# Kernel tuning notes

Hardware: AMD Instinct MI355X
Metric: run time of the kernel (lower is better)

## Reference

```python
import jax, jax.numpy as jnp
import numpy as np

D_MODEL = 1024
NUM_HEADS = 16
HEAD_DIM = D_MODEL // NUM_HEADS


def setup_inputs() -> dict:
    key = jax.random.key(0)
    k_x, k_wqkv, k_bqkv, k_wo, k_bo = jax.random.split(key, 5)
    B, T = 2, 2048
    bound_qkv = 1.0 / np.sqrt(D_MODEL)
    bound_o = 1.0 / np.sqrt(D_MODEL)
    return {
        "x": jax.random.normal(k_x, (B, T, D_MODEL), dtype=jnp.float32),
        # stored as (in, out) for clean x @ W
        "w_qkv": jax.random.uniform(k_wqkv, (D_MODEL, 3 * D_MODEL), jnp.float32, -bound_qkv, bound_qkv),
        "b_qkv": jax.random.uniform(k_bqkv, (3 * D_MODEL,), jnp.float32, -bound_qkv, bound_qkv),
        "w_out": jax.random.uniform(k_wo, (D_MODEL, D_MODEL), jnp.float32, -bound_o, bound_o),
        "b_out": jax.random.uniform(k_bo, (D_MODEL,), jnp.float32, -bound_o, bound_o),
    }


def reference(x, w_qkv, b_qkv, w_out, b_out):
    B, T, C = x.shape
    H, Dh = NUM_HEADS, HEAD_DIM
    scale = jnp.sqrt(jnp.asarray(Dh, dtype=x.dtype))
    qkv = x @ w_qkv + b_qkv                      # [B, T, 3C]
    q, k, v = jnp.split(qkv, 3, axis=-1)         # each [B, T, C]
    # [B, T, C] -> [B, H, T, Dh]
    q = q.reshape(B, T, H, Dh).transpose(0, 2, 1, 3)
    k = k.reshape(B, T, H, Dh).transpose(0, 2, 1, 3)
    v = v.reshape(B, T, H, Dh).transpose(0, 2, 1, 3)
    scores = jnp.einsum("bhqd,bhkd->bhqk", q, k) / scale   # [B, H, T, T]
    probs = jax.nn.softmax(scores, axis=-1)
    attn = jnp.einsum("bhqk,bhkd->bhqd", probs, v)          # [B, H, T, Dh]
    attn = attn.transpose(0, 2, 1, 3).reshape(B, T, C)
    return attn @ w_out + b_out
```

## Files before the change

### kernel.cpp

```cpp
#include <hip/hip_runtime.h>
#include <stdint.h>

typedef __bf16 bf16x8 __attribute__((ext_vector_type(8)));
typedef float f32x4 __attribute__((ext_vector_type(4)));
typedef float f32x16 __attribute__((ext_vector_type(16)));
typedef unsigned short u16x8 __attribute__((ext_vector_type(8)));

#define D_MODEL 1024
#define T_SEQ 2048
#define BATCH 2
#define NHEAD 16
#define HDIM 64
#define MROWS (BATCH * T_SEQ)
#define HEADS_TOTAL (BATCH * NHEAD)
#define QKV_ELEMS (HEADS_TOTAL * T_SEQ * HDIM)

__device__ __forceinline__ unsigned short f32_to_bf16_rne(float f) {
    uint32_t u = __builtin_bit_cast(uint32_t, f);
    uint32_t r = (u + 0x7FFFu + ((u >> 16) & 1u)) >> 16;
    return (unsigned short)r;
}

__device__ __forceinline__ uint32_t pack2(float a, float b) {
    return (uint32_t)f32_to_bf16_rne(a) | ((uint32_t)f32_to_bf16_rne(b) << 16);
}

__device__ __forceinline__ void gload_lds16(const void* g, void* l) {
    __builtin_amdgcn_global_load_lds(
        (const __attribute__((address_space(1))) void*)g,
        (__attribute__((address_space(3))) void*)l, 16, 0, 0);
}

__device__ __forceinline__ f32x4 mfma_bf16(bf16x8 a, bf16x8 b, f32x4 c) {
    return __builtin_amdgcn_mfma_f32_16x16x32_bf16(a, b, c, 0, 0, 0);
}
__device__ __forceinline__ f32x16 mfma32(bf16x8 a, bf16x8 b, f32x16 c) {
    return __builtin_amdgcn_mfma_f32_32x32x16_bf16(a, b, c, 0, 0, 0);
}

__global__ void k_convert(const float4* __restrict__ in, u16x8* __restrict__ out, int n8) {
    int i = blockIdx.x * 256 + threadIdx.x;
    if (i >= n8) return;
    float4 a = in[i * 2];
    float4 b = in[i * 2 + 1];
    u16x8 r;
    r[0] = f32_to_bf16_rne(a.x); r[1] = f32_to_bf16_rne(a.y);
    r[2] = f32_to_bf16_rne(a.z); r[3] = f32_to_bf16_rne(a.w);
    r[4] = f32_to_bf16_rne(b.x); r[5] = f32_to_bf16_rne(b.y);
    r[6] = f32_to_bf16_rne(b.z); r[7] = f32_to_bf16_rne(b.w);
    out[i] = r;
}

__global__ void k_transpose_conv(const float* __restrict__ in, unsigned short* __restrict__ out,
                                 int R, int C) {
    __shared__ float tile[32][33];
    int nc = C >> 5;
    int tc0 = (blockIdx.x % nc) * 32;
    int tr0 = (blockIdx.x / nc) * 32;
    int tx = threadIdx.x & 31, ty = threadIdx.x >> 5;
#pragma unroll
    for (int i = 0; i < 4; ++i) {
        int r = ty * 4 + i;
        tile[r][tx] = in[(size_t)(tr0 + r) * C + tc0 + tx];
    }
    __syncthreads();
#pragma unroll
    for (int i = 0; i < 4; ++i) {
        int c = ty * 4 + i;
        out[(size_t)(tc0 + c) * R + tr0 + tx] = f32_to_bf16_rne(tile[tx][c]);
    }
}

template <int EPI>
__global__ __launch_bounds__(256) void k_gemm(const unsigned short* __restrict__ A,
                                              const unsigned short* __restrict__ Bt,
                                              const float* __restrict__ bias,
                                              void* __restrict__ outp,
                                              int M, int N, int K) {
    __shared__ __align__(16) unsigned short As[128 * 32];
    __shared__ __align__(16) unsigned short Bs[128 * 32];
    const int NB = N >> 7;
    int bm = blockIdx.x / NB, bn = blockIdx.x % NB;
    int tid = threadIdx.x;
    int lane = tid & 63, w = tid >> 6;
    int wr = w >> 1, wc = w & 1;
    int l15 = lane & 15, lg = lane >> 4;

    f32x4 acc[4][4] = {};

    const int nK = K >> 5;
    int c1 = tid, c2 = tid + 256;
    int r1 = c1 >> 2, o1 = (c1 & 3) * 8;
    int r2 = c2 >> 2, o2 = (c2 & 3) * 8;
    char* AsB = (char*)As;
    char* BsB = (char*)Bs;

    for (int kt = 0; kt < nK; ++kt) {
        if (kt) __syncthreads();
        int k0 = kt * 32;
        gload_lds16(A + (size_t)(bm * 128 + r1) * K + k0 + o1, AsB + w * 1024);
        gload_lds16(A + (size_t)(bm * 128 + r2) * K + k0 + o2, AsB + 4096 + w * 1024);
        gload_lds16(Bt + (size_t)(bn * 128 + r1) * K + k0 + o1, BsB + w * 1024);
        gload_lds16(Bt + (size_t)(bn * 128 + r2) * K + k0 + o2, BsB + 4096 + w * 1024);
        __syncthreads();

        bf16x8 af[4], bfr[4];
#pragma unroll
        for (int i = 0; i < 4; ++i)
            af[i] = *(const bf16x8*)(As + (wr * 64 + i * 16 + l15) * 32 + lg * 8);
#pragma unroll
        for (int j = 0; j < 4; ++j)
            bfr[j] = *(const bf16x8*)(Bs + (wc * 64 + j * 16 + l15) * 32 + lg * 8);
#pragma unroll
        for (int i = 0; i < 4; ++i)
#pragma unroll
            for (int j = 0; j < 4; ++j)
                acc[i][j] = mfma_bf16(af[i], bfr[j], acc[i][j]);
    }

    if (EPI == 1) {
        float* out = (float*)outp;
#pragma unroll
        for (int jn = 0; jn < 4; ++jn) {
            int n = bn * 128 + wc * 64 + jn * 16 + l15;
            float bv = bias[n];
#pragma unroll
            for (int i = 0; i < 4; ++i) {
#pragma unroll
                for (int j = 0; j < 4; ++j) {
                    int m = bm * 128 + wr * 64 + i * 16 + lg * 4 + j;
                    out[(size_t)m * N + n] = acc[i][jn][j] + bv;
                }
            }
        }
    } else {
        unsigned short* qkv = (unsigned short*)outp;
#pragma unroll
        for (int jn = 0; jn < 4; ++jn) {
            int n = bn * 128 + wc * 64 + jn * 16 + l15;
            float bv = bias[n];
            int part = n >> 10;
            int cc = n & 1023;
            int h = cc >> 6, d = cc & 63;
            float scale = (part == 0) ? 0.125f : 1.0f;
            unsigned short* dst = qkv + (size_t)part * QKV_ELEMS;
#pragma unroll
            for (int i = 0; i < 4; ++i) {
#pragma unroll
                for (int j = 0; j < 4; ++j) {
                    int m = bm * 128 + wr * 64 + i * 16 + lg * 4 + j;
                    int b = m >> 11, t = m & 2047;
                    float v = (acc[i][jn][j] + bv) * scale;
                    dst[((size_t)(b * NHEAD + h) * T_SEQ + t) * HDIM + d] = f32_to_bf16_rne(v);
                }
            }
        }
    }
}

__global__ void k_transpose_v(const unsigned short* __restrict__ V, unsigned short* __restrict__ Vt) {
    __shared__ unsigned short tile[64][66];
    int bh = blockIdx.x >> 5;
    int t0 = (blockIdx.x & 31) * 64;
    const unsigned short* Vb = V + (size_t)bh * T_SEQ * HDIM;
    unsigned short* Vtb = Vt + (size_t)bh * HDIM * T_SEQ;
    int d = threadIdx.x & 63, tq = threadIdx.x >> 6;
#pragma unroll
    for (int r = 0; r < 16; ++r) {
        int tl = tq * 16 + r;
        tile[tl][d] = Vb[(size_t)(t0 + tl) * HDIM + d];
    }
    __syncthreads();
    int tl = threadIdx.x & 63, dq = threadIdx.x >> 6;
#pragma unroll
    for (int r = 0; r < 16; ++r) {
        int dd = dq * 16 + r;
        Vtb[(size_t)dd * T_SEQ + t0 + tl] = tile[tl][dd];
    }
}

__global__ __launch_bounds__(256) void k_attn(const unsigned short* __restrict__ Qg,
                                              const unsigned short* __restrict__ Kg,
                                              const unsigned short* __restrict__ Vtg,
                                              unsigned short* __restrict__ Og) {
    __shared__ __align__(16) unsigned short Ks[2][64 * 64];
    __shared__ __align__(16) unsigned short Vs[2][64 * 64];
    __shared__ __align__(16) unsigned short Pl[4][32 * 64];

    const int NT = T_SEQ / 64;
    int bid = blockIdx.x;
    int idx = bid >> 3;
    int bh = (bid & 7) * 4 + (idx >> 4);
    int qt = idx & 15;
    int tid = threadIdx.x;
    int w = tid >> 6, lane = tid & 63;
    int l31 = lane & 31, hi = lane >> 5;
    int r7 = l31 & 7;

    const unsigned short* Qb = Qg + (size_t)bh * T_SEQ * HDIM;
    const unsigned short* Kb = Kg + (size_t)bh * T_SEQ * HDIM;
    const unsigned short* Vb = Vtg + (size_t)bh * HDIM * T_SEQ;

    int q0 = qt * 128 + w * 32;

    bf16x8 qf[4];
#pragma unroll
    for (int ks = 0; ks < 4; ++ks)
        qf[ks] = *(const bf16x8*)(Qb + (size_t)(q0 + l31) * HDIM + ks * 16 + hi * 8);

    f32x16 o_[2] = {};
    float m = -INFINITY, l = 0.f;
    char* pB = (char*)Pl[w];

#define STAGE(tile, buf)                                                             \
    do {                                                                             \
        int kv0s = (tile) * 64;                                                      \
        _Pragma("unroll") for (int i_ = 0; i_ < 2; ++i_) {                           \
            int c_ = i_ * 256 + tid;                                                 \
            int row_ = c_ >> 3;                                                      \
            int cs_ = (c_ & 7) ^ (row_ & 7);                                         \
            gload_lds16(Kb + (size_t)(kv0s + row_) * HDIM + cs_ * 8,                 \
                        (char*)Ks[buf] + i_ * 4096 + w * 1024);                      \
            gload_lds16(Vb + (size_t)row_ * T_SEQ + kv0s + cs_ * 8,                  \
                        (char*)Vs[buf] + i_ * 4096 + w * 1024);                      \
        }                                                                            \
    } while (0)

    STAGE(0, 0);
    __syncthreads();

    for (int t = 0; t < NT; ++t) {
        int cur = t & 1;
        if (t + 1 < NT) STAGE(t + 1, cur ^ 1);

        const char* Kt = (const char*)Ks[cur];
        const char* Vt_ = (const char*)Vs[cur];

        f32x16 s_[2] = {};
#pragma unroll
        for (int ti = 0; ti < 2; ++ti) {
            int row = ti * 32 + l31;
#pragma unroll
            for (int ks = 0; ks < 4; ++ks) {
                bf16x8 kf = *(const bf16x8*)(Kt + row * 128 + ((((ks << 1) | hi) ^ r7) << 4));
                s_[ti] = mfma32(kf, qf[ks], s_[ti]);
            }
        }

        float mx = -INFINITY;
#pragma unroll
        for (int ti = 0; ti < 2; ++ti)
#pragma unroll
            for (int rr = 0; rr < 16; ++rr) mx = fmaxf(mx, s_[ti][rr]);
        mx = fmaxf(mx, __shfl_xor(mx, 32));
        float mn = fmaxf(m, mx);
        float sc = __expf(m - mn);
        m = mn;
        float ps = 0.f;
#pragma unroll
        for (int ti = 0; ti < 2; ++ti)
#pragma unroll
            for (int rr = 0; rr < 16; ++rr) {
                float e = __expf(s_[ti][rr] - mn);
                s_[ti][rr] = e;
                ps += e;
            }
        ps += __shfl_xor(ps, 32);
        l = l * sc + ps;
#pragma unroll
        for (int rr = 0; rr < 16; ++rr) {
            o_[0][rr] *= sc;
            o_[1][rr] *= sc;
        }

#pragma unroll
        for (int ti = 0; ti < 2; ++ti)
#pragma unroll
            for (int g = 0; g < 4; ++g) {
                uint32_t w0 = pack2(s_[ti][4 * g], s_[ti][4 * g + 1]);
                uint32_t w1 = pack2(s_[ti][4 * g + 2], s_[ti][4 * g + 3]);
                int c16 = (ti * 4 + g) ^ r7;
                *(uint2*)(pB + l31 * 128 + c16 * 16 + hi * 8) = make_uint2(w0, w1);
            }
        asm volatile("s_waitcnt lgkmcnt(0)" ::: "memory");
        bf16x8 pa[4];
#pragma unroll
        for (int ks = 0; ks < 4; ++ks)
            pa[ks] = *(const bf16x8*)(pB + l31 * 128 + ((((ks << 1) | hi) ^ r7) << 4));

#pragma unroll
        for (int dn = 0; dn < 2; ++dn) {
            int row = dn * 32 + l31;
#pragma unroll
            for (int ks = 0; ks < 4; ++ks) {
                bf16x8 vf = *(const bf16x8*)(Vt_ + row * 128 + ((((ks << 1) | hi) ^ r7) << 4));
                o_[dn] = mfma32(vf, pa[ks], o_[dn]);
            }
        }
        __syncthreads();
    }
#undef STAGE

    float inv = 1.0f / l;
#pragma unroll
    for (int rr = 0; rr < 16; ++rr) {
        o_[0][rr] *= inv;
        o_[1][rr] *= inv;
    }
#pragma unroll
    for (int dn = 0; dn < 2; ++dn)
#pragma unroll
        for (int g = 0; g < 4; ++g) {
            uint32_t w0 = pack2(o_[dn][4 * g], o_[dn][4 * g + 1]);
            uint32_t w1 = pack2(o_[dn][4 * g + 2], o_[dn][4 * g + 3]);
            int c16 = (dn * 4 + g) ^ r7;
            *(uint2*)(pB + l31 * 128 + c16 * 16 + hi * 8) = make_uint2(w0, w1);
        }
    asm volatile("s_waitcnt lgkmcnt(0)" ::: "memory");
    int b = bh >> 4, h = bh & 15;
#pragma unroll
    for (int i = 0; i < 4; ++i) {
        int c = i * 64 + lane;
        int row = c >> 3;
        int c16l = c & 7;
        bf16x8 ov = *(const bf16x8*)(pB + row * 128 + ((c16l ^ (row & 7)) << 4));
        *(bf16x8*)(Og + ((size_t)(b * T_SEQ + q0 + row)) * D_MODEL + h * HDIM + c16l * 8) = ov;
    }
}

extern "C" void kernel_launch(void* const* d_in, const int* in_sizes, int n_in,
                              void* d_out, int out_size, void* d_ws, size_t ws_size,
                              hipStream_t stream) {
    const float* x = (const float*)d_in[0];
    const float* w_qkv = (const float*)d_in[1];
    const float* b_qkv = (const float*)d_in[2];
    const float* w_out = (const float*)d_in[3];
    const float* b_out = (const float*)d_in[4];
    float* out = (float*)d_out;
    char* ws = (char*)d_ws;

    unsigned short* x_bf   = (unsigned short*)(ws + 0);
    unsigned short* wqkv_t = (unsigned short*)(ws + 8388608);
    unsigned short* wout_t = (unsigned short*)(ws + 14680064);
    unsigned short* Qb     = (unsigned short*)(ws + 16777216);
    unsigned short* Kb     = (unsigned short*)(ws + 25165824);
    unsigned short* Vb     = (unsigned short*)(ws + 33554432);
    unsigned short* Vt     = x_bf;
    unsigned short* Ob     = Vb;

    k_convert<<<MROWS * D_MODEL / 8 / 256, 256, 0, stream>>>((const float4*)x, (u16x8*)x_bf,
                                                             MROWS * D_MODEL / 8);
    k_transpose_conv<<<(D_MODEL / 32) * (3 * D_MODEL / 32), 256, 0, stream>>>(w_qkv, wqkv_t,
                                                                              D_MODEL, 3 * D_MODEL);
    k_transpose_conv<<<(D_MODEL / 32) * (D_MODEL / 32), 256, 0, stream>>>(w_out, wout_t,
                                                                          D_MODEL, D_MODEL);
    k_gemm<0><<<(MROWS / 128) * (3 * D_MODEL / 128), 256, 0, stream>>>(x_bf, wqkv_t, b_qkv,
                                                                       (void*)Qb, MROWS,
                                                                       3 * D_MODEL, D_MODEL);
    k_transpose_v<<<HEADS_TOTAL * (T_SEQ / 64), 256, 0, stream>>>(Vb, Vt);
    k_attn<<<512, 256, 0, stream>>>(Qb, Kb, Vt, Ob);
    k_gemm<1><<<(MROWS / 128) * (D_MODEL / 128), 256, 0, stream>>>(Ob, wout_t, b_out, (void*)out,
                                                                   MROWS, D_MODEL, D_MODEL);
}
```

Before: 229.3 us.

## Double-buffer GEMM tiles, use exp2 softmax with lazy rescale, shuffle P in registers

The GEMM kernel now double-buffers its LDS tiles, prefetching the next K-slice while the current one feeds the MFMAs, with one barrier per iteration. The attention kernel folds log2(e) into the Q scale so it can use exp2, replaces the serial max/sum reductions with tree reductions, and only rescales the running max and accumulators when the max grows by more than 8. The P matrix is repacked into MFMA operand layout with cross-half lane shuffles instead of a round trip through LDS, which removes the per-warp P buffer. The epilogue reuses the K buffer, and the lazy rescale relies on bounded growth of the exponentials in fp32.

```diff
diff --git a/kernel.cpp b/kernel.cpp
--- a/kernel.cpp
+++ b/kernel.cpp
@@ -5,6 +5,7 @@
 typedef float f32x4 __attribute__((ext_vector_type(4)));
 typedef float f32x16 __attribute__((ext_vector_type(16)));
 typedef unsigned short u16x8 __attribute__((ext_vector_type(8)));
+typedef uint32_t u32x4 __attribute__((ext_vector_type(4)));
 
 #define D_MODEL 1024
 #define T_SEQ 2048
@@ -14,6 +15,8 @@
 #define MROWS (BATCH * T_SEQ)
 #define HEADS_TOTAL (BATCH * NHEAD)
 #define QKV_ELEMS (HEADS_TOTAL * T_SEQ * HDIM)
+
+#define QSCALE_LOG2 0.1803368801111204f
 
 __device__ __forceinline__ unsigned short f32_to_bf16_rne(float f) {
     uint32_t u = __builtin_bit_cast(uint32_t, f);
@@ -77,8 +80,8 @@
                                               const float* __restrict__ bias,
                                               void* __restrict__ outp,
                                               int M, int N, int K) {
-    __shared__ __align__(16) unsigned short As[128 * 32];
-    __shared__ __align__(16) unsigned short Bs[128 * 32];
+    __shared__ __align__(16) unsigned short As[2][128 * 32];
+    __shared__ __align__(16) unsigned short Bs[2][128 * 32];
     const int NB = N >> 7;
     int bm = blockIdx.x / NB, bn = blockIdx.x % NB;
     int tid = threadIdx.x;
@@ -92,31 +95,44 @@
     int c1 = tid, c2 = tid + 256;
     int r1 = c1 >> 2, o1 = (c1 & 3) * 8;
     int r2 = c2 >> 2, o2 = (c2 & 3) * 8;
-    char* AsB = (char*)As;
-    char* BsB = (char*)Bs;
+
+#define GSTAGE(kt, buf)                                                          \
+    do {                                                                         \
+        int k0_ = (kt) * 32;                                                     \
+        gload_lds16(A + (size_t)(bm * 128 + r1) * K + k0_ + o1,                  \
+                    (char*)As[buf] + w * 1024);                                  \
+        gload_lds16(A + (size_t)(bm * 128 + r2) * K + k0_ + o2,                  \
+                    (char*)As[buf] + 4096 + w * 1024);                           \
+        gload_lds16(Bt + (size_t)(bn * 128 + r1) * K + k0_ + o1,                 \
+                    (char*)Bs[buf] + w * 1024);                                  \
+        gload_lds16(Bt + (size_t)(bn * 128 + r2) * K + k0_ + o2,                 \
+                    (char*)Bs[buf] + 4096 + w * 1024);                           \
+    } while (0)
+
+    GSTAGE(0, 0);
+    __syncthreads();
 
     for (int kt = 0; kt < nK; ++kt) {
-        if (kt) __syncthreads();
-        int k0 = kt * 32;
-        gload_lds16(A + (size_t)(bm * 128 + r1) * K + k0 + o1, AsB + w * 1024);
-        gload_lds16(A + (size_t)(bm * 128 + r2) * K + k0 + o2, AsB + 4096 + w * 1024);
-        gload_lds16(Bt + (size_t)(bn * 128 + r1) * K + k0 + o1, BsB + w * 1024);
-        gload_lds16(Bt + (size_t)(bn * 128 + r2) * K + k0 + o2, BsB + 4096 + w * 1024);
-        __syncthreads();
-
+        int cur = kt & 1;
+        if (kt + 1 < nK) GSTAGE(kt + 1, cur ^ 1);
+
+        const unsigned short* Ac = As[cur];
+        const unsigned short* Bc = Bs[cur];
         bf16x8 af[4], bfr[4];
 #pragma unroll
         for (int i = 0; i < 4; ++i)
-            af[i] = *(const bf16x8*)(As + (wr * 64 + i * 16 + l15) * 32 + lg * 8);
+            af[i] = *(const bf16x8*)(Ac + (wr * 64 + i * 16 + l15) * 32 + lg * 8);
 #pragma unroll
         for (int j = 0; j < 4; ++j)
-            bfr[j] = *(const bf16x8*)(Bs + (wc * 64 + j * 16 + l15) * 32 + lg * 8);
+            bfr[j] = *(const bf16x8*)(Bc + (wc * 64 + j * 16 + l15) * 32 + lg * 8);
 #pragma unroll
         for (int i = 0; i < 4; ++i)
 #pragma unroll
             for (int j = 0; j < 4; ++j)
                 acc[i][j] = mfma_bf16(af[i], bfr[j], acc[i][j]);
-    }
+        __syncthreads();
+    }
+#undef GSTAGE
 
     if (EPI == 1) {
         float* out = (float*)outp;
@@ -142,7 +158,7 @@
             int part = n >> 10;
             int cc = n & 1023;
             int h = cc >> 6, d = cc & 63;
-            float scale = (part == 0) ? 0.125f : 1.0f;
+            float scale = (part == 0) ? QSCALE_LOG2 : 1.0f;
             unsigned short* dst = qkv + (size_t)part * QKV_ELEMS;
 #pragma unroll
             for (int i = 0; i < 4; ++i) {
@@ -185,7 +201,6 @@
                                               unsigned short* __restrict__ Og) {
     __shared__ __align__(16) unsigned short Ks[2][64 * 64];
     __shared__ __align__(16) unsigned short Vs[2][64 * 64];
-    __shared__ __align__(16) unsigned short Pl[4][32 * 64];
 
     const int NT = T_SEQ / 64;
     int bid = blockIdx.x;
@@ -210,7 +225,6 @@
 
     f32x16 o_[2] = {};
     float m = -INFINITY, l = 0.f;
-    char* pB = (char*)Pl[w];
 
 #define STAGE(tile, buf)                                                             \
     do {                                                                             \
@@ -247,46 +261,61 @@
             }
         }
 
-        float mx = -INFINITY;
+        float t16[16];
+#pragma unroll
+        for (int rr = 0; rr < 16; ++rr) t16[rr] = fmaxf(s_[0][rr], s_[1][rr]);
+#pragma unroll
+        for (int st = 8; st >= 1; st >>= 1)
+#pragma unroll
+            for (int rr = 0; rr < 8; ++rr)
+                if (rr < st) t16[rr] = fmaxf(t16[rr], t16[rr + st]);
+        float mx = fmaxf(t16[0], __shfl_xor(t16[0], 32));
+
+        if (__any(mx - m > 8.0f)) {
+            float mn = fmaxf(m, mx);
+            float sc = __builtin_exp2f(m - mn);
+            m = mn;
+            l *= sc;
+#pragma unroll
+            for (int rr = 0; rr < 16; ++rr) {
+                o_[0][rr] *= sc;
+                o_[1][rr] *= sc;
+            }
+        }
+
+        float a16[16];
 #pragma unroll
         for (int ti = 0; ti < 2; ++ti)
 #pragma unroll
-            for (int rr = 0; rr < 16; ++rr) mx = fmaxf(mx, s_[ti][rr]);
-        mx = fmaxf(mx, __shfl_xor(mx, 32));
-        float mn = fmaxf(m, mx);
-        float sc = __expf(m - mn);
-        m = mn;
-        float ps = 0.f;
-#pragma unroll
-        for (int ti = 0; ti < 2; ++ti)
-#pragma unroll
-            for (int rr = 0; rr < 16; ++rr) {
-                float e = __expf(s_[ti][rr] - mn);
-                s_[ti][rr] = e;
-                ps += e;
-            }
-        ps += __shfl_xor(ps, 32);
-        l = l * sc + ps;
-#pragma unroll
-        for (int rr = 0; rr < 16; ++rr) {
-            o_[0][rr] *= sc;
-            o_[1][rr] *= sc;
-        }
-
-#pragma unroll
-        for (int ti = 0; ti < 2; ++ti)
-#pragma unroll
-            for (int g = 0; g < 4; ++g) {
-                uint32_t w0 = pack2(s_[ti][4 * g], s_[ti][4 * g + 1]);
-                uint32_t w1 = pack2(s_[ti][4 * g + 2], s_[ti][4 * g + 3]);
-                int c16 = (ti * 4 + g) ^ r7;
-                *(uint2*)(pB + l31 * 128 + c16 * 16 + hi * 8) = make_uint2(w0, w1);
-            }
-        asm volatile("s_waitcnt lgkmcnt(0)" ::: "memory");
+            for (int rr = 0; rr < 16; ++rr) s_[ti][rr] = __builtin_exp2f(s_[ti][rr] - m);
+#pragma unroll
+        for (int rr = 0; rr < 16; ++rr) a16[rr] = s_[0][rr] + s_[1][rr];
+#pragma unroll
+        for (int st = 8; st >= 1; st >>= 1)
+#pragma unroll
+            for (int rr = 0; rr < 8; ++rr)
+                if (rr < st) a16[rr] += a16[rr + st];
+        l += a16[0] + __shfl_xor(a16[0], 32);
+
         bf16x8 pa[4];
 #pragma unroll
-        for (int ks = 0; ks < 4; ++ks)
-            pa[ks] = *(const bf16x8*)(pB + l31 * 128 + ((((ks << 1) | hi) ^ r7) << 4));
+        for (int ks = 0; ks < 4; ++ks) {
+            int ti = ks >> 1, k1 = ks & 1;
+            uint32_t PA = pack2(s_[ti][8 * k1 + 0], s_[ti][8 * k1 + 1]);
+            uint32_t PC = pack2(s_[ti][8 * k1 + 2], s_[ti][8 * k1 + 3]);
+            uint32_t PB = pack2(s_[ti][8 * k1 + 4], s_[ti][8 * k1 + 5]);
+            uint32_t PD = pack2(s_[ti][8 * k1 + 6], s_[ti][8 * k1 + 7]);
+            uint32_t u0 = hi ? PA : PB;
+            uint32_t u1 = hi ? PC : PD;
+            uint32_t x0 = (uint32_t)__shfl_xor((int)u0, 32);
+            uint32_t x1 = (uint32_t)__shfl_xor((int)u1, 32);
+            u32x4 ww;
+            ww[0] = hi ? x0 : PA;
+            ww[1] = hi ? x1 : PC;
+            ww[2] = hi ? PB : x0;
+            ww[3] = hi ? PD : x1;
+            pa[ks] = __builtin_bit_cast(bf16x8, ww);
+        }
 
 #pragma unroll
         for (int dn = 0; dn < 2; ++dn) {
@@ -307,6 +336,7 @@
         o_[0][rr] *= inv;
         o_[1][rr] *= inv;
     }
+    char* eB = (char*)Ks + (size_t)w * 4096;
 #pragma unroll
     for (int dn = 0; dn < 2; ++dn)
 #pragma unroll
@@ -314,7 +344,7 @@
             uint32_t w0 = pack2(o_[dn][4 * g], o_[dn][4 * g + 1]);
             uint32_t w1 = pack2(o_[dn][4 * g + 2], o_[dn][4 * g + 3]);
             int c16 = (dn * 4 + g) ^ r7;
-            *(uint2*)(pB + l31 * 128 + c16 * 16 + hi * 8) = make_uint2(w0, w1);
+            *(uint2*)(eB + l31 * 128 + c16 * 16 + hi * 8) = make_uint2(w0, w1);
         }
     asm volatile("s_waitcnt lgkmcnt(0)" ::: "memory");
     int b = bh >> 4, h = bh & 15;
@@ -323,7 +353,7 @@
         int c = i * 64 + lane;
         int row = c >> 3;
         int c16l = c & 7;
-        bf16x8 ov = *(const bf16x8*)(pB + row * 128 + ((c16l ^ (row & 7)) << 4));
+        bf16x8 ov = *(const bf16x8*)(eB + row * 128 + ((c16l ^ (row & 7)) << 4));
         *(bf16x8*)(Og + ((size_t)(b * T_SEQ + q0 + row)) * D_MODEL + h * HDIM + c16l * 8) = ov;
     }
 }
```

New measurement: 250.8 us. 1.09x slower.
